# Optimization experiments

Measured on AMD Instinct MI355X. Metric: run time of the kernel, lower is better.

Reference implementation:

```python
import jax, jax.numpy as jnp
import numpy as np

N_NODES = 100000
N_EDGES = 1600000
D_FEAT = 64


def setup_inputs() -> dict:
    key = jax.random.key(0)
    k1, k2, k3, k4 = jax.random.split(key, 4)
    rows = jnp.sort(jax.random.randint(k1, (N_EDGES,), 0, N_NODES, dtype=jnp.int64))
    cols = jax.random.randint(k2, (N_EDGES,), 0, N_NODES, dtype=jnp.int64)
    vals = jax.random.uniform(k3, (N_EDGES,), dtype=jnp.float32)
    embeds = jax.random.normal(k4, (N_NODES, D_FEAT), dtype=jnp.float32)
    return {"rows": rows, "cols": cols, "vals": vals, "embeds": embeds}


def reference(rows, cols, vals, embeds):
    # out[i] = sum_{e: rows[e]==i} vals[e] * embeds[cols[e]]  (torch.spmm with COO adj)
    gathered = vals[:, None] * embeds[cols]          # [E, d]
    out = jax.ops.segment_sum(gathered, rows, num_segments=N_NODES)  # [N, d]
    return out
```

## Files before the change

### kernel.cpp

```cpp
#include <hip/hip_runtime.h>
#include <hip/hip_bf16.h>


constexpr int D = 64;

__device__ __forceinline__ unsigned bf16rnd(unsigned u) {
    return (u + 0x7FFFu + ((u >> 16) & 1u)) >> 16;
}

__global__ __launch_bounds__(256) void cvt_kernel(
    const uint4* __restrict__ src,
    uint4* __restrict__ dst,
    int n8)
{
    int i = blockIdx.x * blockDim.x + threadIdx.x;
    if (i >= n8) return;
    uint4 a = src[2 * i];
    uint4 b = src[2 * i + 1];
    uint4 o;
    o.x = bf16rnd(a.x) | (bf16rnd(a.y) << 16);
    o.y = bf16rnd(a.z) | (bf16rnd(a.w) << 16);
    o.z = bf16rnd(b.x) | (bf16rnd(b.y) << 16);
    o.w = bf16rnd(b.z) | (bf16rnd(b.w) << 16);
    dst[i] = o;
}

__global__ __launch_bounds__(256) void rowptr_kernel(
    const int* __restrict__ rows, int* __restrict__ row_ptr,
    int n_edges, int n_nodes)
{
    int e = blockIdx.x * blockDim.x + threadIdx.x;
    if (e >= n_edges) return;
    int r_cur  = rows[e];
    int r_prev = (e == 0) ? -1 : rows[e - 1];
    for (int r = r_prev + 1; r <= r_cur; ++r) row_ptr[r] = e;
    if (e == n_edges - 1)
        for (int r = r_cur + 1; r <= n_nodes; ++r) row_ptr[r] = n_edges;
}

__device__ __forceinline__ float bflo(unsigned w) {
    union { unsigned u; float f; } x; x.u = w << 16; return x.f;
}
__device__ __forceinline__ float bfhi(unsigned w) {
    union { unsigned u; float f; } x; x.u = w & 0xFFFF0000u; return x.f;
}

__global__ __launch_bounds__(256) void spmm_node_kernel(
    const int* __restrict__ row_ptr,
    const int* __restrict__ cols,
    const float* __restrict__ vals,
    const uint2* __restrict__ ebf,
    float4* __restrict__ out4,
    int n_nodes)
{
    const int lane = threadIdx.x & 63;
    const int t    = lane & 15;
    const int s    = lane >> 4;
    const int wave = blockIdx.x * (blockDim.x >> 6) + (threadIdx.x >> 6);
    const int node = wave * 4 + s;
    if (node >= n_nodes) return;

    const int lo = row_ptr[node];
    const int hi = row_ptr[node + 1];

    float4 acc = make_float4(0.f, 0.f, 0.f, 0.f);

    for (int e = lo; e < hi; e += 8) {
        const int last = hi - 1;
        int i0 = e;
        int i1 = (e + 1 <= last) ? e + 1 : last;
        int i2 = (e + 2 <= last) ? e + 2 : last;
        int i3 = (e + 3 <= last) ? e + 3 : last;
        int i4 = (e + 4 <= last) ? e + 4 : last;
        int i5 = (e + 5 <= last) ? e + 5 : last;
        int i6 = (e + 6 <= last) ? e + 6 : last;
        int i7 = (e + 7 <= last) ? e + 7 : last;

        int c0 = cols[i0], c1 = cols[i1], c2 = cols[i2], c3 = cols[i3];
        int c4 = cols[i4], c5 = cols[i5], c6 = cols[i6], c7 = cols[i7];

        float v0 = vals[i0];
        float v1 = (e + 1 < hi) ? vals[i1] : 0.f;
        float v2 = (e + 2 < hi) ? vals[i2] : 0.f;
        float v3 = (e + 3 < hi) ? vals[i3] : 0.f;
        float v4 = (e + 4 < hi) ? vals[i4] : 0.f;
        float v5 = (e + 5 < hi) ? vals[i5] : 0.f;
        float v6 = (e + 6 < hi) ? vals[i6] : 0.f;
        float v7 = (e + 7 < hi) ? vals[i7] : 0.f;

        uint2 m0 = ebf[c0 * 16 + t];
        uint2 m1 = ebf[c1 * 16 + t];
        uint2 m2 = ebf[c2 * 16 + t];
        uint2 m3 = ebf[c3 * 16 + t];
        uint2 m4 = ebf[c4 * 16 + t];
        uint2 m5 = ebf[c5 * 16 + t];
        uint2 m6 = ebf[c6 * 16 + t];
        uint2 m7 = ebf[c7 * 16 + t];

        acc.x += v0 * bflo(m0.x); acc.y += v0 * bfhi(m0.x);
        acc.z += v0 * bflo(m0.y); acc.w += v0 * bfhi(m0.y);
        acc.x += v1 * bflo(m1.x); acc.y += v1 * bfhi(m1.x);
        acc.z += v1 * bflo(m1.y); acc.w += v1 * bfhi(m1.y);
        acc.x += v2 * bflo(m2.x); acc.y += v2 * bfhi(m2.x);
        acc.z += v2 * bflo(m2.y); acc.w += v2 * bfhi(m2.y);
        acc.x += v3 * bflo(m3.x); acc.y += v3 * bfhi(m3.x);
        acc.z += v3 * bflo(m3.y); acc.w += v3 * bfhi(m3.y);
        acc.x += v4 * bflo(m4.x); acc.y += v4 * bfhi(m4.x);
        acc.z += v4 * bflo(m4.y); acc.w += v4 * bfhi(m4.y);
        acc.x += v5 * bflo(m5.x); acc.y += v5 * bfhi(m5.x);
        acc.z += v5 * bflo(m5.y); acc.w += v5 * bfhi(m5.y);
        acc.x += v6 * bflo(m6.x); acc.y += v6 * bfhi(m6.x);
        acc.z += v6 * bflo(m6.y); acc.w += v6 * bfhi(m6.y);
        acc.x += v7 * bflo(m7.x); acc.y += v7 * bfhi(m7.x);
        acc.z += v7 * bflo(m7.y); acc.w += v7 * bfhi(m7.y);
    }

    out4[(long)node * 16 + t] = acc;
}

extern "C" void kernel_launch(void* const* d_in, const int* in_sizes, int n_in,
                              void* d_out, int out_size, void* d_ws, size_t ws_size,
                              hipStream_t stream) {
    const int*   rows   = (const int*)d_in[0];
    const int*   cols   = (const int*)d_in[1];
    const float* vals   = (const float*)d_in[2];
    const float* embeds = (const float*)d_in[3];
    float4*      out4   = (float4*)d_out;

    const int n_edges = in_sizes[0];
    const int n_nodes = out_size / D;
    const int n_feat  = in_sizes[3];

    char* ws = (char*)d_ws;
    uint4* ebf_table = (uint4*)ws;
    int*   row_ptr   = (int*)(ws + (size_t)n_feat * 2);

    int n8 = n_feat / 8;
    cvt_kernel<<<(n8 + 255) / 256, 256, 0, stream>>>(
        (const uint4*)embeds, ebf_table, n8);

    rowptr_kernel<<<(n_edges + 255) / 256, 256, 0, stream>>>(
        rows, row_ptr, n_edges, n_nodes);

    int waves  = (n_nodes + 3) / 4;
    int blocks = (waves + 3) / 4;
    spmm_node_kernel<<<blocks, 256, 0, stream>>>(
        row_ptr, cols, vals, (const uint2*)ebf_table, out4, n_nodes);
}
```

Baseline: 127.6 us.

## Merge prep kernels into one launch and gather 16-byte bf16 rows per lane

The bf16 conversion and row-pointer construction kernels are merged into one launch that splits work by block index. This removes a kernel launch and lets the two independent prep jobs run concurrently. The SpMM kernel now uses 8 lanes per node, each loading a 16-byte uint4 (8 bf16 features), so a wave covers 8 nodes. The edge unroll drops from 8 to 4 to keep registers in check, which means fewer gathers are in flight per lane, though each gather is wider.

```diff
diff --git a/kernel.cpp b/kernel.cpp
--- a/kernel.cpp
+++ b/kernel.cpp
@@ -8,34 +8,33 @@
     return (u + 0x7FFFu + ((u >> 16) & 1u)) >> 16;
 }
 
-__global__ __launch_bounds__(256) void cvt_kernel(
+__global__ __launch_bounds__(256) void prep_kernel(
     const uint4* __restrict__ src,
     uint4* __restrict__ dst,
-    int n8)
+    int n8,
+    const int* __restrict__ rows, int* __restrict__ row_ptr,
+    int n_edges, int n_nodes, int cvt_blocks)
 {
-    int i = blockIdx.x * blockDim.x + threadIdx.x;
-    if (i >= n8) return;
-    uint4 a = src[2 * i];
-    uint4 b = src[2 * i + 1];
-    uint4 o;
-    o.x = bf16rnd(a.x) | (bf16rnd(a.y) << 16);
-    o.y = bf16rnd(a.z) | (bf16rnd(a.w) << 16);
-    o.z = bf16rnd(b.x) | (bf16rnd(b.y) << 16);
-    o.w = bf16rnd(b.z) | (bf16rnd(b.w) << 16);
-    dst[i] = o;
-}
-
-__global__ __launch_bounds__(256) void rowptr_kernel(
-    const int* __restrict__ rows, int* __restrict__ row_ptr,
-    int n_edges, int n_nodes)
-{
-    int e = blockIdx.x * blockDim.x + threadIdx.x;
-    if (e >= n_edges) return;
-    int r_cur  = rows[e];
-    int r_prev = (e == 0) ? -1 : rows[e - 1];
-    for (int r = r_prev + 1; r <= r_cur; ++r) row_ptr[r] = e;
-    if (e == n_edges - 1)
-        for (int r = r_cur + 1; r <= n_nodes; ++r) row_ptr[r] = n_edges;
+    if ((int)blockIdx.x < cvt_blocks) {
+        int i = blockIdx.x * 256 + threadIdx.x;
+        if (i >= n8) return;
+        uint4 a = src[2 * i];
+        uint4 b = src[2 * i + 1];
+        uint4 o;
+        o.x = bf16rnd(a.x) | (bf16rnd(a.y) << 16);
+        o.y = bf16rnd(a.z) | (bf16rnd(a.w) << 16);
+        o.z = bf16rnd(b.x) | (bf16rnd(b.y) << 16);
+        o.w = bf16rnd(b.z) | (bf16rnd(b.w) << 16);
+        dst[i] = o;
+    } else {
+        int e = (blockIdx.x - cvt_blocks) * 256 + threadIdx.x;
+        if (e >= n_edges) return;
+        int r_cur  = rows[e];
+        int r_prev = (e == 0) ? -1 : rows[e - 1];
+        for (int r = r_prev + 1; r <= r_cur; ++r) row_ptr[r] = e;
+        if (e == n_edges - 1)
+            for (int r = r_cur + 1; r <= n_nodes; ++r) row_ptr[r] = n_edges;
+    }
 }
 
 __device__ __forceinline__ float bflo(unsigned w) {
@@ -49,73 +48,66 @@
     const int* __restrict__ row_ptr,
     const int* __restrict__ cols,
     const float* __restrict__ vals,
-    const uint2* __restrict__ ebf,
+    const uint4* __restrict__ ebf4,
     float4* __restrict__ out4,
     int n_nodes)
 {
     const int lane = threadIdx.x & 63;
-    const int t    = lane & 15;
-    const int s    = lane >> 4;
+    const int t    = lane & 7;
+    const int s    = lane >> 3;
     const int wave = blockIdx.x * (blockDim.x >> 6) + (threadIdx.x >> 6);
-    const int node = wave * 4 + s;
+    const int node = wave * 8 + s;
     if (node >= n_nodes) return;
 
     const int lo = row_ptr[node];
     const int hi = row_ptr[node + 1];
 
-    float4 acc = make_float4(0.f, 0.f, 0.f, 0.f);
+    float4 acc0 = make_float4(0.f, 0.f, 0.f, 0.f);
+    float4 acc1 = make_float4(0.f, 0.f, 0.f, 0.f);
 
-    for (int e = lo; e < hi; e += 8) {
+    for (int e = lo; e < hi; e += 4) {
         const int last = hi - 1;
         int i0 = e;
         int i1 = (e + 1 <= last) ? e + 1 : last;
         int i2 = (e + 2 <= last) ? e + 2 : last;
         int i3 = (e + 3 <= last) ? e + 3 : last;
-        int i4 = (e + 4 <= last) ? e + 4 : last;
-        int i5 = (e + 5 <= last) ? e + 5 : last;
-        int i6 = (e + 6 <= last) ? e + 6 : last;
-        int i7 = (e + 7 <= last) ? e + 7 : last;
 
         int c0 = cols[i0], c1 = cols[i1], c2 = cols[i2], c3 = cols[i3];
-        int c4 = cols[i4], c5 = cols[i5], c6 = cols[i6], c7 = cols[i7];
 
         float v0 = vals[i0];
         float v1 = (e + 1 < hi) ? vals[i1] : 0.f;
         float v2 = (e + 2 < hi) ? vals[i2] : 0.f;
         float v3 = (e + 3 < hi) ? vals[i3] : 0.f;
-        float v4 = (e + 4 < hi) ? vals[i4] : 0.f;
-        float v5 = (e + 5 < hi) ? vals[i5] : 0.f;
-        float v6 = (e + 6 < hi) ? vals[i6] : 0.f;
-        float v7 = (e + 7 < hi) ? vals[i7] : 0.f;
 
-        uint2 m0 = ebf[c0 * 16 + t];
-        uint2 m1 = ebf[c1 * 16 + t];
-        uint2 m2 = ebf[c2 * 16 + t];
-        uint2 m3 = ebf[c3 * 16 + t];
-        uint2 m4 = ebf[c4 * 16 + t];
-        uint2 m5 = ebf[c5 * 16 + t];
-        uint2 m6 = ebf[c6 * 16 + t];
-        uint2 m7 = ebf[c7 * 16 + t];
+        uint4 m0 = ebf4[c0 * 8 + t];
+        uint4 m1 = ebf4[c1 * 8 + t];
+        uint4 m2 = ebf4[c2 * 8 + t];
+        uint4 m3 = ebf4[c3 * 8 + t];
 
-        acc.x += v0 * bflo(m0.x); acc.y += v0 * bfhi(m0.x);
-        acc.z += v0 * bflo(m0.y); acc.w += v0 * bfhi(m0.y);
-        acc.x += v1 * bflo(m1.x); acc.y += v1 * bfhi(m1.x);
-        acc.z += v1 * bflo(m1.y); acc.w += v1 * bfhi(m1.y);
-        acc.x += v2 * bflo(m2.x); acc.y += v2 * bfhi(m2.x);
-        acc.z += v2 * bflo(m2.y); acc.w += v2 * bfhi(m2.y);
-        acc.x += v3 * bflo(m3.x); acc.y += v3 * bfhi(m3.x);
-        acc.z += v3 * bflo(m3.y); acc.w += v3 * bfhi(m3.y);
-        acc.x += v4 * bflo(m4.x); acc.y += v4 * bfhi(m4.x);
-        acc.z += v4 * bflo(m4.y); acc.w += v4 * bfhi(m4.y);
-        acc.x += v5 * bflo(m5.x); acc.y += v5 * bfhi(m5.x);
-        acc.z += v5 * bflo(m5.y); acc.w += v5 * bfhi(m5.y);
-        acc.x += v6 * bflo(m6.x); acc.y += v6 * bfhi(m6.x);
-        acc.z += v6 * bflo(m6.y); acc.w += v6 * bfhi(m6.y);
-        acc.x += v7 * bflo(m7.x); acc.y += v7 * bfhi(m7.x);
-        acc.z += v7 * bflo(m7.y); acc.w += v7 * bfhi(m7.y);
+        acc0.x += v0 * bflo(m0.x); acc0.y += v0 * bfhi(m0.x);
+        acc0.z += v0 * bflo(m0.y); acc0.w += v0 * bfhi(m0.y);
+        acc1.x += v0 * bflo(m0.z); acc1.y += v0 * bfhi(m0.z);
+        acc1.z += v0 * bflo(m0.w); acc1.w += v0 * bfhi(m0.w);
+
+        acc0.x += v1 * bflo(m1.x); acc0.y += v1 * bfhi(m1.x);
+        acc0.z += v1 * bflo(m1.y); acc0.w += v1 * bfhi(m1.y);
+        acc1.x += v1 * bflo(m1.z); acc1.y += v1 * bfhi(m1.z);
+        acc1.z += v1 * bflo(m1.w); acc1.w += v1 * bfhi(m1.w);
+
+        acc0.x += v2 * bflo(m2.x); acc0.y += v2 * bfhi(m2.x);
+        acc0.z += v2 * bflo(m2.y); acc0.w += v2 * bfhi(m2.y);
+        acc1.x += v2 * bflo(m2.z); acc1.y += v2 * bfhi(m2.z);
+        acc1.z += v2 * bflo(m2.w); acc1.w += v2 * bfhi(m2.w);
+
+        acc0.x += v3 * bflo(m3.x); acc0.y += v3 * bfhi(m3.x);
+        acc0.z += v3 * bflo(m3.y); acc0.w += v3 * bfhi(m3.y);
+        acc1.x += v3 * bflo(m3.z); acc1.y += v3 * bfhi(m3.z);
+        acc1.z += v3 * bflo(m3.w); acc1.w += v3 * bfhi(m3.w);
     }
 
-    out4[(long)node * 16 + t] = acc;
+    long ob = (long)node * 16 + 2 * t;
+    out4[ob]     = acc0;
+    out4[ob + 1] = acc1;
 }
 
 extern "C" void kernel_launch(void* const* d_in, const int* in_sizes, int n_in,
@@ -131,19 +123,19 @@
     const int n_nodes = out_size / D;
     const int n_feat  = in_sizes[3];
 
-    char* ws = (char*)d_ws;
+    char*  ws        = (char*)d_ws;
     uint4* ebf_table = (uint4*)ws;
     int*   row_ptr   = (int*)(ws + (size_t)n_feat * 2);
 
-    int n8 = n_feat / 8;
-    cvt_kernel<<<(n8 + 255) / 256, 256, 0, stream>>>(
-        (const uint4*)embeds, ebf_table, n8);
+    int n8         = n_feat / 8;
+    int cvt_blocks = (n8 + 255) / 256;
+    int row_blocks = (n_edges + 255) / 256;
+    prep_kernel<<<cvt_blocks + row_blocks, 256, 0, stream>>>(
+        (const uint4*)embeds, ebf_table, n8,
+        rows, row_ptr, n_edges, n_nodes, cvt_blocks);
 
-    rowptr_kernel<<<(n_edges + 255) / 256, 256, 0, stream>>>(
-        rows, row_ptr, n_edges, n_nodes);
-
-    int waves  = (n_nodes + 3) / 4;
+    int waves  = (n_nodes + 7) / 8;
     int blocks = (waves + 3) / 4;
     spmm_node_kernel<<<blocks, 256, 0, stream>>>(
-        row_ptr, cols, vals, (const uint2*)ebf_table, out4, n_nodes);
+        row_ptr, cols, vals, ebf_table, out4, n_nodes);
 }
```

Measured after the change: 122.2 us. -4.2%, faster.
